# Performance work log

Measured on AMD Instinct MI355X. Metric: run time of the kernel, lower is better.

Reference implementation:

```python
import jax, jax.numpy as jnp
import numpy as np

N_AGENTS = 32
UNIT_DIM = 32
STATE_DIM = 1200
N_HEAD = 8
EMBED = 64
KEY_HID = 2 * EMBED
HYPER = 256
V_HID = 4 * EMBED
ATTEND_REG_COEF = 0.001
BS, T = 128, 32


def setup_inputs() -> dict:
    key = jax.random.key(0)
    ks = jax.random.split(key, 12)
    def lin(k, shape, fan_in):
        return jax.random.normal(k, shape, jnp.float32) / np.sqrt(fan_in)
    return dict(
        agent_qs=jax.random.normal(ks[0], (BS, T, N_AGENTS), jnp.float32),
        states=jax.random.normal(ks[1], (BS, T, STATE_DIM), jnp.float32),
        actions=jax.random.randint(ks[2], (BS, T, N_AGENTS), 0, 20),
        sel_W1=lin(ks[3], (N_HEAD, HYPER, STATE_DIM), STATE_DIM),
        sel_b1=jnp.zeros((N_HEAD, HYPER), jnp.float32),
        sel_W2=lin(ks[4], (N_HEAD, EMBED, HYPER), HYPER),
        key_W1=lin(ks[5], (N_HEAD, KEY_HID, UNIT_DIM + 1), UNIT_DIM + 1),
        key_b1=jnp.zeros((N_HEAD, KEY_HID), jnp.float32),
        key_W2=lin(ks[6], (N_HEAD, EMBED, KEY_HID), KEY_HID),
        wh_W1=lin(ks[7], (HYPER, STATE_DIM), STATE_DIM),
        wh_b1=jnp.zeros((HYPER,), jnp.float32),
        wh_W2=lin(ks[8], (N_HEAD, HYPER), HYPER),
        wh_b2=jnp.zeros((N_HEAD,), jnp.float32),
        v_W1=lin(ks[9], (V_HID, STATE_DIM), STATE_DIM),
        v_b1=jnp.zeros((V_HID,), jnp.float32),
        v_W2=lin(ks[10], (1, V_HID), V_HID),
        v_b2=jnp.zeros((1,), jnp.float32),
    )


def reference(agent_qs, states, actions, sel_W1, sel_b1, sel_W2, key_W1, key_b1, key_W2,
              wh_W1, wh_b1, wh_W2, wh_b2, v_W1, v_b1, v_W2, v_b2):
    bs = agent_qs.shape[0]
    s = states.reshape(-1, STATE_DIM)                       # (B, S), B = bs*T
    B = s.shape[0]
    units = s[:, :UNIT_DIM * N_AGENTS].reshape(B, N_AGENTS, UNIT_DIM)  # (B, A, U)
    q = agent_qs.reshape(B, N_AGENTS)                       # (B, A)
    # nonlinear=True: append each agent's q to its unit features
    units = jnp.concatenate([units, q[:, :, None]], axis=2)  # (B, A, U+1)
    a = actions.reshape(B, N_AGENTS)
    # selector hypernets (all heads batched): (B, H, E)
    h1 = jax.nn.relu(jnp.einsum('bs,hes->bhe', s, sel_W1) + sel_b1[None])
    sel = jnp.einsum('bhe,hde->bhd', h1, sel_W2)
    # key hypernets (all heads x all agents batched): (B, H, A, E)
    k1 = jax.nn.relu(jnp.einsum('bau,hku->bhak', units, key_W1) + key_b1[None, :, None, :])
    keys = jnp.einsum('bhak,hdk->bhad', k1, key_W2)
    logits = jnp.einsum('bhd,bhad->bha', sel, keys)          # unscaled, used for regularizer
    scaled = logits / np.sqrt(EMBED)
    scaled = jnp.where(a[:, None, :] == 0, -99999999.0, scaled)  # mask_dead
    w = jax.nn.softmax(scaled, axis=2)                       # (B, H, A)
    head_q = jnp.einsum('ba,bha->bh', q, w)                  # (B, H)
    # weighted_head + state_bias
    wh = jnp.abs(jax.nn.relu(s @ wh_W1.T + wh_b1) @ wh_W2.T + wh_b2)  # (B, H)
    v = (jax.nn.relu(s @ v_W1.T + v_b1) @ v_W2.T + v_b2)[:, 0]        # (B,)
    y = (wh * head_q).sum(axis=1) + v
    q_tot = y.reshape(bs, -1, 1)
    # sum over heads of per-head mean of squared (unscaled) logits
    attend_mag_regs = ATTEND_REG_COEF * (logits ** 2).mean(axis=(0, 2)).sum()
    # per-head entropy: sum over agents, mean over batch
    head_entropies = -(jnp.log(w + 1e-8) * w).sum(axis=2).mean(axis=0)  # (H,)
    return q_tot, attend_mag_regs, head_entropies
```

## Files before the change

### kernel.cpp

```cpp
#include <hip/hip_runtime.h>

#define B_TOT 4096
#define SDIM  1200
#define KPAD  1216
#define NA    32
#define NH    8
#define EMB   64
#define KHID  128
#define HYP   256
#define NSEL  2048
#define NTOT  2560

#define WS_H1BF 0
#define WS_M    (WS_H1BF + (size_t)B_TOT * NTOT / 2)
#define WS_LG   (WS_M    + (size_t)B_TOT * NH * KHID)
#define WS_PART (WS_LG   + (size_t)B_TOT * NH * NA)
#define WS_P2   (WS_PART + (size_t)B_TOT * 16)
#define WS_ABF  (WS_P2   + (size_t)32 * 16)
#define WS_WBF  (WS_ABF  + (size_t)B_TOT * KPAD / 2)
#define WS_KW32 (WS_WBF  + (size_t)NTOT * KPAD / 2)
#define WS_W32F (WS_KW32 + (size_t)1024 * 32 / 2)
#define WS_M2T  (WS_W32F + (size_t)1024)
#define WS_UBF  (WS_M2T  + (size_t)NH * KHID * HYP / 2)

typedef __attribute__((ext_vector_type(8))) short short8v;
typedef __attribute__((ext_vector_type(4))) float floatx4;

#define GLL16(gsrc, ldst) __builtin_amdgcn_global_load_lds( \
    (const __attribute__((address_space(1))) unsigned int*)(gsrc), \
    (__attribute__((address_space(3))) unsigned int*)(ldst), 16, 0, 0)

__device__ __forceinline__ ushort f2bf(float x) {
    unsigned u = __builtin_bit_cast(unsigned, x);
    unsigned r = (u + 0x7FFFu + ((u >> 16) & 1u)) >> 16;
    return (ushort)r;
}
__device__ __forceinline__ float bf2f(ushort u) {
    unsigned x = ((unsigned)u) << 16;
    return __builtin_bit_cast(float, x);
}

__global__ __launch_bounds__(256) void k_cvt_states(
    const float* __restrict__ src, ushort* __restrict__ dst)
{
    const size_t g = (size_t)blockIdx.x * 256 + threadIdx.x;
    if (g >= (size_t)B_TOT * (KPAD / 4)) return;
    const int row = (int)(g / (KPAD / 4));
    const int c4  = (int)(g % (KPAD / 4)) * 4;
    ushort4 o = {0, 0, 0, 0};
    if (c4 < SDIM) {
        float4 v = *(const float4*)(src + (size_t)row * SDIM + c4);
        o.x = f2bf(v.x); o.y = f2bf(v.y); o.z = f2bf(v.z); o.w = f2bf(v.w);
    }
    *(ushort4*)(dst + (size_t)row * KPAD + c4) = o;
}

__global__ __launch_bounds__(256) void k_cvt_w(
    const float* __restrict__ sel_W1, const float* __restrict__ wh_W1,
    const float* __restrict__ v_W1, ushort* __restrict__ dst)
{
    const size_t g = (size_t)blockIdx.x * 256 + threadIdx.x;
    if (g >= (size_t)NTOT * (KPAD / 4)) return;
    const int row = (int)(g / (KPAD / 4));
    const int c4  = (int)(g % (KPAD / 4)) * 4;
    const float* src = (row < NSEL)       ? (sel_W1 + (size_t)row * SDIM)
                     : (row < NSEL + HYP) ? (wh_W1 + (size_t)(row - NSEL) * SDIM)
                                          : (v_W1  + (size_t)(row - NSEL - HYP) * SDIM);
    ushort4 o = {0, 0, 0, 0};
    if (c4 < SDIM) {
        float4 v = *(const float4*)(src + c4);
        o.x = f2bf(v.x); o.y = f2bf(v.y); o.z = f2bf(v.z); o.w = f2bf(v.w);
    }
    *(ushort4*)(dst + (size_t)row * KPAD + c4) = o;
}

__global__ __launch_bounds__(256) void k_cvt_units(
    const float* __restrict__ states, ushort* __restrict__ dst)
{
    const int row = blockIdx.x * 256 + threadIdx.x;
    if (row >= B_TOT * NA) return;
    const int b = row >> 5, a = row & 31;
    const float* s = states + (size_t)b * SDIM + a * 32;
    ushort o[32];
    #pragma unroll
    for (int j = 0; j < 8; ++j) {
        float4 v = *(const float4*)(s + j * 4);
        o[j * 4 + 0] = f2bf(v.x); o[j * 4 + 1] = f2bf(v.y);
        o[j * 4 + 2] = f2bf(v.z); o[j * 4 + 3] = f2bf(v.w);
    }
    #pragma unroll
    for (int c = 0; c < 4; ++c)
        *(short8v*)(dst + (size_t)row * 32 + c * 8) = *(short8v*)&o[c * 8];
}

__global__ __launch_bounds__(256) void k_cvt_kw2(
    const float* __restrict__ key_W1, ushort* __restrict__ kw32,
    float* __restrict__ w32f)
{
    const int row = blockIdx.x * 256 + threadIdx.x;
    if (row >= 1024) return;
    const float* srcr = key_W1 + (size_t)row * 33;
    ushort o[32];
    #pragma unroll
    for (int u = 0; u < 32; ++u) o[u] = f2bf(srcr[u]);
    #pragma unroll
    for (int c = 0; c < 4; ++c)
        *(short8v*)(kw32 + (size_t)row * 32 + c * 8) = *(short8v*)&o[c * 8];
    w32f[row] = srcr[32];
}

__global__ __launch_bounds__(256) void k_m2(
    const float* __restrict__ sel_W2, const float* __restrict__ key_W2,
    ushort* __restrict__ M2T)
{
    __shared__ float ssel[EMB * HYP];
    __shared__ float skey[EMB][8];
    const int t  = threadIdx.x;
    const int h  = blockIdx.x;
    const int k0 = blockIdx.y * 8;

    const float4* sw = (const float4*)(sel_W2 + (size_t)h * EMB * HYP);
    #pragma unroll
    for (int j = 0; j < 16; ++j)
        ((float4*)ssel)[j * 256 + t] = sw[j * 256 + t];
    if (t < EMB) {
        #pragma unroll
        for (int kk = 0; kk < 8; ++kk)
            skey[t][kk] = key_W2[((size_t)h * EMB + t) * KHID + k0 + kk];
    }
    __syncthreads();

    const int e = t;
    float acc[8] = {};
    for (int d = 0; d < EMB; ++d) {
        const float sv = ssel[d * HYP + e];
        #pragma unroll
        for (int kk = 0; kk < 8; ++kk)
            acc[kk] = fmaf(sv, skey[d][kk], acc[kk]);
    }
    #pragma unroll
    for (int kk = 0; kk < 8; ++kk)
        M2T[((size_t)h * KHID + k0 + kk) * HYP + e] = f2bf(acc[kk]);
}

#define BK 32
__global__ __launch_bounds__(256) void k_gemm1_mfma(
    const ushort* __restrict__ Abf, const ushort* __restrict__ Wbf,
    const float* __restrict__ sel_b1, const float* __restrict__ wh_b1,
    const float* __restrict__ v_b1, ushort* __restrict__ h1bf)
{
    __shared__ ushort As[128 * BK];
    __shared__ ushort Bs[128 * BK];
    const int tid = threadIdx.x;
    const int l   = tid & 63;
    const int w   = tid >> 6;
    const int wM  = w >> 1, wN = w & 1;
    const int arow0 = blockIdx.y * 128;
    const int nrow0 = blockIdx.x * 128;

    const int srow = tid >> 2;
    const int skof = (tid & 3) * 8;
    const ushort* gA = Abf + (size_t)(arow0 + srow) * KPAD + skof;
    const ushort* gB = Wbf + (size_t)(nrow0 + srow) * KPAD + skof;
    ushort* lA = &As[srow * BK + skof];
    ushort* lB = &Bs[srow * BK + skof];

    floatx4 acc[4][4] = {};

    for (int k0 = 0; k0 < KPAD; k0 += BK) {
        GLL16(gA + k0, lA);
        GLL16(gA + (size_t)64 * KPAD + k0, lA + 64 * BK);
        GLL16(gB + k0, lB);
        GLL16(gB + (size_t)64 * KPAD + k0, lB + 64 * BK);
        __syncthreads();

        const int kch = (l >> 4) * 8;
        short8v av[4], bv[4];
        #pragma unroll
        for (int mi = 0; mi < 4; ++mi)
            av[mi] = *(const short8v*)&As[(wM * 64 + mi * 16 + (l & 15)) * BK + kch];
        #pragma unroll
        for (int ni = 0; ni < 4; ++ni)
            bv[ni] = *(const short8v*)&Bs[(wN * 64 + ni * 16 + (l & 15)) * BK + kch];
        #pragma unroll
        for (int mi = 0; mi < 4; ++mi)
            #pragma unroll
            for (int ni = 0; ni < 4; ++ni)
                acc[mi][ni] = __builtin_amdgcn_mfma_f32_16x16x32_bf16(
                    av[mi], bv[ni], acc[mi][ni], 0, 0, 0);
        __syncthreads();
    }

    float bias_n[4];
    #pragma unroll
    for (int ni = 0; ni < 4; ++ni) {
        const int col = nrow0 + wN * 64 + ni * 16 + (l & 15);
        bias_n[ni] = (col < NSEL)       ? sel_b1[col]
                   : (col < NSEL + HYP) ? wh_b1[col - NSEL]
                                        : v_b1[col - NSEL - HYP];
    }
    #pragma unroll
    for (int mi = 0; mi < 4; ++mi) {
        const int row = arow0 + wM * 64 + mi * 16 + (l >> 4) * 4;
        #pragma unroll
        for (int ni = 0; ni < 4; ++ni) {
            const int col = nrow0 + wN * 64 + ni * 16 + (l & 15);
            #pragma unroll
            for (int r = 0; r < 4; ++r)
                h1bf[(size_t)(row + r) * NTOT + col] =
                    f2bf(fmaxf(acc[mi][ni][r] + bias_n[ni], 0.f));
        }
    }
}

__global__ __launch_bounds__(256) void k_m_mfma(
    const ushort* __restrict__ h1bf, const ushort* __restrict__ M2T,
    float* __restrict__ m_out)
{
    __shared__ ushort As[128 * BK];
    __shared__ ushort Bs[128 * BK];
    const int tid = threadIdx.x;
    const int l   = tid & 63;
    const int w   = tid >> 6;
    const int wM  = w >> 1, wN = w & 1;
    const int h     = blockIdx.x;
    const int brow0 = blockIdx.y * 128;

    const int srow = tid >> 2;
    const int skof = (tid & 3) * 8;
    const ushort* gA = h1bf + (size_t)(brow0 + srow) * NTOT + h * HYP + skof;
    const ushort* gB = M2T + ((size_t)h * KHID + srow) * HYP + skof;
    ushort* lA = &As[srow * BK + skof];
    ushort* lB = &Bs[srow * BK + skof];

    floatx4 acc[4][4] = {};

    for (int k0 = 0; k0 < HYP; k0 += BK) {
        GLL16(gA + k0, lA);
        GLL16(gA + (size_t)64 * NTOT + k0, lA + 64 * BK);
        GLL16(gB + k0, lB);
        GLL16(gB + (size_t)64 * HYP + k0, lB + 64 * BK);
        __syncthreads();

        const int kch = (l >> 4) * 8;
        short8v av[4], bv[4];
        #pragma unroll
        for (int mi = 0; mi < 4; ++mi)
            av[mi] = *(const short8v*)&As[(wM * 64 + mi * 16 + (l & 15)) * BK + kch];
        #pragma unroll
        for (int ni = 0; ni < 4; ++ni)
            bv[ni] = *(const short8v*)&Bs[(wN * 64 + ni * 16 + (l & 15)) * BK + kch];
        #pragma unroll
        for (int mi = 0; mi < 4; ++mi)
            #pragma unroll
            for (int ni = 0; ni < 4; ++ni)
                acc[mi][ni] = __builtin_amdgcn_mfma_f32_16x16x32_bf16(
                    av[mi], bv[ni], acc[mi][ni], 0, 0, 0);
        __syncthreads();
    }

    #pragma unroll
    for (int mi = 0; mi < 4; ++mi) {
        const int row = brow0 + wM * 64 + mi * 16 + (l >> 4) * 4;
        #pragma unroll
        for (int ni = 0; ni < 4; ++ni) {
            const int col = wN * 64 + ni * 16 + (l & 15);
            #pragma unroll
            for (int r = 0; r < 4; ++r)
                m_out[((size_t)(row + r) * NH + h) * KHID + col] = acc[mi][ni][r];
        }
    }
}

__global__ __launch_bounds__(256) void k_logits_mfma(
    const ushort* __restrict__ Ubf, const ushort* __restrict__ KW32,
    const float* __restrict__ W32f, const float* __restrict__ key_b1,
    const float* __restrict__ agent_qs, const float* __restrict__ m_in,
    float* __restrict__ logits)
{
    const int tid = threadIdx.x;
    const int l   = tid & 63;
    const int w   = tid >> 6;
    const int b   = blockIdx.x * 4 + w;
    const int urow0 = b * NA;

    short8v av[2];
    float4 qv[2];
    #pragma unroll
    for (int mi = 0; mi < 2; ++mi) {
        av[mi] = *(const short8v*)(
            Ubf + (size_t)(urow0 + mi * 16 + (l & 15)) * 32 + (l >> 4) * 8);
        qv[mi] = *(const float4*)(
            agent_qs + (size_t)b * NA + mi * 16 + (l >> 4) * 4);
    }

    for (int h = 0; h < NH; ++h) {
        short8v bv[8];
        float b1r[8], w32r[8], mr[8];
        #pragma unroll
        for (int ni = 0; ni < 8; ++ni) {
            const int k = ni * 16 + (l & 15);
            bv[ni]   = *(const short8v*)(
                KW32 + ((size_t)h * KHID + k) * 32 + (l >> 4) * 8);
            b1r[ni]  = key_b1[h * KHID + k];
            w32r[ni] = W32f[h * KHID + k];
            mr[ni]   = m_in[((size_t)b * NH + h) * KHID + k];
        }
        floatx4 acc[2][8] = {};
        #pragma unroll
        for (int mi = 0; mi < 2; ++mi)
            #pragma unroll
            for (int ni = 0; ni < 8; ++ni)
                acc[mi][ni] = __builtin_amdgcn_mfma_f32_16x16x32_bf16(
                    av[mi], bv[ni], acc[mi][ni], 0, 0, 0);

        #pragma unroll
        for (int mi = 0; mi < 2; ++mi) {
            float s0 = 0.f, s1 = 0.f, s2 = 0.f, s3 = 0.f;
            #pragma unroll
            for (int ni = 0; ni < 8; ++ni) {
                const float b1v = b1r[ni], wv = w32r[ni], mv = mr[ni];
                s0 = fmaf(fmaxf(fmaf(qv[mi].x, wv, acc[mi][ni][0] + b1v), 0.f), mv, s0);
                s1 = fmaf(fmaxf(fmaf(qv[mi].y, wv, acc[mi][ni][1] + b1v), 0.f), mv, s1);
                s2 = fmaf(fmaxf(fmaf(qv[mi].z, wv, acc[mi][ni][2] + b1v), 0.f), mv, s2);
                s3 = fmaf(fmaxf(fmaf(qv[mi].w, wv, acc[mi][ni][3] + b1v), 0.f), mv, s3);
            }
            #pragma unroll
            for (int off = 8; off >= 1; off >>= 1) {
                s0 += __shfl_xor(s0, off);
                s1 += __shfl_xor(s1, off);
                s2 += __shfl_xor(s2, off);
                s3 += __shfl_xor(s3, off);
            }
            if ((l & 15) == 0) {
                float4 o = {s0, s1, s2, s3};
                *(float4*)(logits + ((size_t)b * NH + h) * NA
                           + mi * 16 + (l >> 4) * 4) = o;
            }
        }
    }
}

__global__ __launch_bounds__(256) void k_softmax(
    const float* __restrict__ logits, const float* __restrict__ agent_qs,
    const int* __restrict__ actions, const ushort* __restrict__ h1bf,
    const float* __restrict__ wh_W2, const float* __restrict__ wh_b2,
    const float* __restrict__ v_W2, const float* __restrict__ v_b2,
    float* __restrict__ out, float* __restrict__ part)
{
    __shared__ float qs[NA];
    __shared__ int   act_s[NA];
    __shared__ float whs[NH];
    __shared__ float hq[NH];
    __shared__ float vred[4];
    const int b = blockIdx.x, t = threadIdx.x;
    if (t < NA) {
        qs[t]    = agent_qs[(size_t)b * NA + t];
        act_s[t] = actions[(size_t)b * NA + t];
    }
    const int h = t >> 5, a = t & 31;
    {
        float acc = 0.f;
        #pragma unroll
        for (int j = 0; j < 8; ++j) {
            const int e = a + 32 * j;
            acc = fmaf(bf2f(h1bf[(size_t)b * NTOT + NSEL + e]),
                       wh_W2[h * HYP + e], acc);
        }
        #pragma unroll
        for (int off = 16; off >= 1; off >>= 1) acc += __shfl_xor(acc, off, 32);
        if (a == 0) whs[h] = fabsf(acc + wh_b2[h]);
    }
    {
        float acc = bf2f(h1bf[(size_t)b * NTOT + NSEL + HYP + t]) * v_W2[t];
        #pragma unroll
        for (int off = 32; off >= 1; off >>= 1) acc += __shfl_xor(acc, off);
        if ((t & 63) == 0) vred[t >> 6] = acc;
    }
    __syncthreads();

    const float lg = logits[((size_t)b * NH + h) * NA + a];
    float sc = (act_s[a] == 0) ? -99999999.0f : lg * 0.125f;

    float mx = sc;
    #pragma unroll
    for (int off = 16; off >= 1; off >>= 1) mx = fmaxf(mx, __shfl_xor(mx, off, 32));
    const float e = expf(sc - mx);
    float sum = e;
    #pragma unroll
    for (int off = 16; off >= 1; off >>= 1) sum += __shfl_xor(sum, off, 32);
    const float wgt = e / sum;

    float r_sq  = lg * lg;
    float r_hq  = qs[a] * wgt;
    float r_ent = -wgt * logf(wgt + 1e-8f);
    #pragma unroll
    for (int off = 16; off >= 1; off >>= 1) {
        r_sq  += __shfl_xor(r_sq,  off, 32);
        r_hq  += __shfl_xor(r_hq,  off, 32);
        r_ent += __shfl_xor(r_ent, off, 32);
    }
    if (a == 0) {
        hq[h] = r_hq;
        part[(size_t)b * 16 + h]     = r_sq;
        part[(size_t)b * 16 + 8 + h] = r_ent;
    }
    __syncthreads();
    if (t == 0) {
        float y = vred[0] + vred[1] + vred[2] + vred[3] + v_b2[0];
        #pragma unroll
        for (int i = 0; i < NH; ++i) y = fmaf(whs[i], hq[i], y);
        out[b] = y;
    }
}

__global__ __launch_bounds__(256) void k_final_s1(
    const float* __restrict__ part, float* __restrict__ part2)
{
    __shared__ float red[16][17];
    const int t = threadIdx.x;
    const int c = t & 15, rl = t >> 4;
    const int rbase = blockIdx.x * 128 + rl;
    float v0 = 0.f, v1 = 0.f, v2 = 0.f, v3 = 0.f;
    #pragma unroll
    for (int j = 0; j < 8; j += 4) {
        v0 += part[(size_t)(rbase + (j + 0) * 16) * 16 + c];
        v1 += part[(size_t)(rbase + (j + 1) * 16) * 16 + c];
        v2 += part[(size_t)(rbase + (j + 2) * 16) * 16 + c];
        v3 += part[(size_t)(rbase + (j + 3) * 16) * 16 + c];
    }
    red[rl][c] = (v0 + v1) + (v2 + v3);
    __syncthreads();
    if (t < 16) {
        float s = 0.f;
        #pragma unroll
        for (int i = 0; i < 16; ++i) s += red[i][t];
        part2[blockIdx.x * 16 + t] = s;
    }
}

__global__ __launch_bounds__(256) void k_final_s2(
    const float* __restrict__ part2, float* __restrict__ out)
{
    __shared__ float red[16][17];
    __shared__ float tot[16];
    const int t = threadIdx.x;
    {
        const int g = t >> 4, c = t & 15;
        red[g][c] = part2[t] + part2[t + 256];
    }
    __syncthreads();
    if (t < 16) {
        float s = 0.f;
        #pragma unroll
        for (int i = 0; i < 16; ++i) s += red[i][t];
        tot[t] = s;
    }
    __syncthreads();
    if (t == 0) {
        float s = 0.f;
        #pragma unroll
        for (int i = 0; i < 8; ++i) s += tot[i];
        out[B_TOT] = 0.001f * (s / (float)((size_t)B_TOT * NA));
    }
    if (t >= 8 && t < 16)
        out[B_TOT + 1 + (t - 8)] = tot[t] / (float)B_TOT;
}

extern "C" void kernel_launch(void* const* d_in, const int* in_sizes, int n_in,
                              void* d_out, int out_size, void* d_ws, size_t ws_size,
                              hipStream_t stream) {
    (void)in_sizes; (void)n_in; (void)out_size; (void)ws_size;
    const float* agent_qs = (const float*)d_in[0];
    const float* states   = (const float*)d_in[1];
    const int*   actions  = (const int*)d_in[2];
    const float* sel_W1   = (const float*)d_in[3];
    const float* sel_b1   = (const float*)d_in[4];
    const float* sel_W2   = (const float*)d_in[5];
    const float* key_W1   = (const float*)d_in[6];
    const float* key_b1   = (const float*)d_in[7];
    const float* key_W2   = (const float*)d_in[8];
    const float* wh_W1    = (const float*)d_in[9];
    const float* wh_b1    = (const float*)d_in[10];
    const float* wh_W2    = (const float*)d_in[11];
    const float* wh_b2    = (const float*)d_in[12];
    const float* v_W1     = (const float*)d_in[13];
    const float* v_b1     = (const float*)d_in[14];
    const float* v_W2     = (const float*)d_in[15];
    const float* v_b2     = (const float*)d_in[16];

    float* out = (float*)d_out;
    float* ws  = (float*)d_ws;
    ushort* h1bf  = (ushort*)(ws + WS_H1BF);
    float* m_buf  = ws + WS_M;
    float* lg_buf = ws + WS_LG;
    float* part   = ws + WS_PART;
    float* part2  = ws + WS_P2;
    ushort* Abf   = (ushort*)(ws + WS_ABF);
    ushort* Wbf   = (ushort*)(ws + WS_WBF);
    ushort* KW32  = (ushort*)(ws + WS_KW32);
    float*  W32f  = ws + WS_W32F;
    ushort* M2T   = (ushort*)(ws + WS_M2T);
    ushort* Ubf   = (ushort*)(ws + WS_UBF);

    {
        const int groups_a = B_TOT * (KPAD / 4);
        const int groups_w = NTOT * (KPAD / 4);
        k_cvt_states<<<(groups_a + 255) / 256, 256, 0, stream>>>(states, Abf);
        k_cvt_w<<<(groups_w + 255) / 256, 256, 0, stream>>>(sel_W1, wh_W1, v_W1, Wbf);
        k_cvt_kw2<<<4, 256, 0, stream>>>(key_W1, KW32, W32f);
        k_cvt_units<<<(B_TOT * NA + 255) / 256, 256, 0, stream>>>(states, Ubf);
        k_m2<<<dim3(NH, KHID / 8), 256, 0, stream>>>(sel_W2, key_W2, M2T);
    }
    k_gemm1_mfma<<<dim3(NTOT / 128, B_TOT / 128), 256, 0, stream>>>(
        Abf, Wbf, sel_b1, wh_b1, v_b1, h1bf);
    k_m_mfma<<<dim3(NH, B_TOT / 128), 256, 0, stream>>>(h1bf, M2T, m_buf);
    k_logits_mfma<<<dim3(B_TOT / 4), 256, 0, stream>>>(
        Ubf, KW32, W32f, key_b1, agent_qs, m_buf, lg_buf);
    k_softmax<<<dim3(B_TOT), 256, 0, stream>>>(
        lg_buf, agent_qs, actions, h1bf, wh_W2, wh_b2, v_W2, v_b2, out, part);
    k_final_s1<<<32, 256, 0, stream>>>(part, part2);
    k_final_s2<<<1, 256, 0, stream>>>(part2, out);
}
```

Before: 123.1 us.

## Double-buffer GEMM LDS tiles, store m in bf16, shrink m tiles, reuse bf16 states

```diff
diff --git a/kernel.cpp b/kernel.cpp
--- a/kernel.cpp
+++ b/kernel.cpp
@@ -12,8 +12,8 @@
 #define NTOT  2560
 
 #define WS_H1BF 0
-#define WS_M    (WS_H1BF + (size_t)B_TOT * NTOT / 2)
-#define WS_LG   (WS_M    + (size_t)B_TOT * NH * KHID)
+#define WS_MBF  (WS_H1BF + (size_t)B_TOT * NTOT / 2)
+#define WS_LG   (WS_MBF  + (size_t)B_TOT * NH * KHID / 2)
 #define WS_PART (WS_LG   + (size_t)B_TOT * NH * NA)
 #define WS_P2   (WS_PART + (size_t)B_TOT * 16)
 #define WS_ABF  (WS_P2   + (size_t)32 * 16)
@@ -75,22 +75,20 @@
 }
 
 __global__ __launch_bounds__(256) void k_cvt_units(
-    const float* __restrict__ states, ushort* __restrict__ dst)
+    const ushort* __restrict__ Abf, ushort* __restrict__ dst)
 {
     const int row = blockIdx.x * 256 + threadIdx.x;
     if (row >= B_TOT * NA) return;
     const int b = row >> 5, a = row & 31;
-    const float* s = states + (size_t)b * SDIM + a * 32;
-    ushort o[32];
-    #pragma unroll
-    for (int j = 0; j < 8; ++j) {
-        float4 v = *(const float4*)(s + j * 4);
-        o[j * 4 + 0] = f2bf(v.x); o[j * 4 + 1] = f2bf(v.y);
-        o[j * 4 + 2] = f2bf(v.z); o[j * 4 + 3] = f2bf(v.w);
-    }
-    #pragma unroll
-    for (int c = 0; c < 4; ++c)
-        *(short8v*)(dst + (size_t)row * 32 + c * 8) = *(short8v*)&o[c * 8];
+    const ushort* s = Abf + (size_t)b * KPAD + a * 32;
+    short8v v0 = *(const short8v*)(s);
+    short8v v1 = *(const short8v*)(s + 8);
+    short8v v2 = *(const short8v*)(s + 16);
+    short8v v3 = *(const short8v*)(s + 24);
+    *(short8v*)(dst + (size_t)row * 32)      = v0;
+    *(short8v*)(dst + (size_t)row * 32 + 8)  = v1;
+    *(short8v*)(dst + (size_t)row * 32 + 16) = v2;
+    *(short8v*)(dst + (size_t)row * 32 + 24) = v3;
 }
 
 __global__ __launch_bounds__(256) void k_cvt_kw2(
@@ -149,8 +147,8 @@
     const float* __restrict__ sel_b1, const float* __restrict__ wh_b1,
     const float* __restrict__ v_b1, ushort* __restrict__ h1bf)
 {
-    __shared__ ushort As[128 * BK];
-    __shared__ ushort Bs[128 * BK];
+    __shared__ ushort As[2][128 * BK];
+    __shared__ ushort Bs[2][128 * BK];
     const int tid = threadIdx.x;
     const int l   = tid & 63;
     const int w   = tid >> 6;
@@ -162,26 +160,30 @@
     const int skof = (tid & 3) * 8;
     const ushort* gA = Abf + (size_t)(arow0 + srow) * KPAD + skof;
     const ushort* gB = Wbf + (size_t)(nrow0 + srow) * KPAD + skof;
-    ushort* lA = &As[srow * BK + skof];
-    ushort* lB = &Bs[srow * BK + skof];
+
+#define STAGE_G1(BUF, KK) do { \
+    GLL16(gA + (KK), &As[BUF][srow * BK + skof]); \
+    GLL16(gA + (size_t)64 * KPAD + (KK), &As[BUF][(64 + srow) * BK + skof]); \
+    GLL16(gB + (KK), &Bs[BUF][srow * BK + skof]); \
+    GLL16(gB + (size_t)64 * KPAD + (KK), &Bs[BUF][(64 + srow) * BK + skof]); \
+} while (0)
 
     floatx4 acc[4][4] = {};
 
+    STAGE_G1(0, 0);
+    __syncthreads();
+    int cur = 0;
     for (int k0 = 0; k0 < KPAD; k0 += BK) {
-        GLL16(gA + k0, lA);
-        GLL16(gA + (size_t)64 * KPAD + k0, lA + 64 * BK);
-        GLL16(gB + k0, lB);
-        GLL16(gB + (size_t)64 * KPAD + k0, lB + 64 * BK);
-        __syncthreads();
+        if (k0 + BK < KPAD) STAGE_G1(cur ^ 1, k0 + BK);
 
         const int kch = (l >> 4) * 8;
         short8v av[4], bv[4];
         #pragma unroll
         for (int mi = 0; mi < 4; ++mi)
-            av[mi] = *(const short8v*)&As[(wM * 64 + mi * 16 + (l & 15)) * BK + kch];
+            av[mi] = *(const short8v*)&As[cur][(wM * 64 + mi * 16 + (l & 15)) * BK + kch];
         #pragma unroll
         for (int ni = 0; ni < 4; ++ni)
-            bv[ni] = *(const short8v*)&Bs[(wN * 64 + ni * 16 + (l & 15)) * BK + kch];
+            bv[ni] = *(const short8v*)&Bs[cur][(wN * 64 + ni * 16 + (l & 15)) * BK + kch];
         #pragma unroll
         for (int mi = 0; mi < 4; ++mi)
             #pragma unroll
@@ -189,6 +191,7 @@
                 acc[mi][ni] = __builtin_amdgcn_mfma_f32_16x16x32_bf16(
                     av[mi], bv[ni], acc[mi][ni], 0, 0, 0);
         __syncthreads();
+        cur ^= 1;
     }
 
     float bias_n[4];
@@ -215,59 +218,64 @@
 
 __global__ __launch_bounds__(256) void k_m_mfma(
     const ushort* __restrict__ h1bf, const ushort* __restrict__ M2T,
-    float* __restrict__ m_out)
-{
-    __shared__ ushort As[128 * BK];
-    __shared__ ushort Bs[128 * BK];
+    ushort* __restrict__ m_out)
+{
+    __shared__ ushort As[2][64 * BK];
+    __shared__ ushort Bs[2][128 * BK];
     const int tid = threadIdx.x;
     const int l   = tid & 63;
     const int w   = tid >> 6;
     const int wM  = w >> 1, wN = w & 1;
     const int h     = blockIdx.x;
-    const int brow0 = blockIdx.y * 128;
+    const int brow0 = blockIdx.y * 64;
 
     const int srow = tid >> 2;
     const int skof = (tid & 3) * 8;
     const ushort* gA = h1bf + (size_t)(brow0 + srow) * NTOT + h * HYP + skof;
     const ushort* gB = M2T + ((size_t)h * KHID + srow) * HYP + skof;
-    ushort* lA = &As[srow * BK + skof];
-    ushort* lB = &Bs[srow * BK + skof];
-
-    floatx4 acc[4][4] = {};
-
+
+#define STAGE_M(BUF, KK) do { \
+    GLL16(gA + (KK), &As[BUF][srow * BK + skof]); \
+    GLL16(gB + (KK), &Bs[BUF][srow * BK + skof]); \
+    GLL16(gB + (size_t)64 * HYP + (KK), &Bs[BUF][(64 + srow) * BK + skof]); \
+} while (0)
+
+    floatx4 acc[2][4] = {};
+
+    STAGE_M(0, 0);
+    __syncthreads();
+    int cur = 0;
     for (int k0 = 0; k0 < HYP; k0 += BK) {
-        GLL16(gA + k0, lA);
-        GLL16(gA + (size_t)64 * NTOT + k0, lA + 64 * BK);
-        GLL16(gB + k0, lB);
-        GLL16(gB + (size_t)64 * HYP + k0, lB + 64 * BK);
-        __syncthreads();
+        if (k0 + BK < HYP) STAGE_M(cur ^ 1, k0 + BK);
 
         const int kch = (l >> 4) * 8;
-        short8v av[4], bv[4];
-        #pragma unroll
-        for (int mi = 0; mi < 4; ++mi)
-            av[mi] = *(const short8v*)&As[(wM * 64 + mi * 16 + (l & 15)) * BK + kch];
+        short8v av[2], bv[4];
+        #pragma unroll
+        for (int mi = 0; mi < 2; ++mi)
+            av[mi] = *(const short8v*)&As[cur][(wM * 32 + mi * 16 + (l & 15)) * BK + kch];
         #pragma unroll
         for (int ni = 0; ni < 4; ++ni)
-            bv[ni] = *(const short8v*)&Bs[(wN * 64 + ni * 16 + (l & 15)) * BK + kch];
-        #pragma unroll
-        for (int mi = 0; mi < 4; ++mi)
+            bv[ni] = *(const short8v*)&Bs[cur][(wN * 64 + ni * 16 + (l & 15)) * BK + kch];
+        #pragma unroll
+        for (int mi = 0; mi < 2; ++mi)
             #pragma unroll
             for (int ni = 0; ni < 4; ++ni)
                 acc[mi][ni] = __builtin_amdgcn_mfma_f32_16x16x32_bf16(
                     av[mi], bv[ni], acc[mi][ni], 0, 0, 0);
         __syncthreads();
-    }
-
-    #pragma unroll
-    for (int mi = 0; mi < 4; ++mi) {
-        const int row = brow0 + wM * 64 + mi * 16 + (l >> 4) * 4;
+        cur ^= 1;
+    }
+
+    #pragma unroll
+    for (int mi = 0; mi < 2; ++mi) {
+        const int row = brow0 + wM * 32 + mi * 16 + (l >> 4) * 4;
         #pragma unroll
         for (int ni = 0; ni < 4; ++ni) {
             const int col = wN * 64 + ni * 16 + (l & 15);
             #pragma unroll
             for (int r = 0; r < 4; ++r)
-                m_out[((size_t)(row + r) * NH + h) * KHID + col] = acc[mi][ni][r];
+                m_out[((size_t)(row + r) * NH + h) * KHID + col] =
+                    f2bf(acc[mi][ni][r]);
         }
     }
 }
@@ -275,7 +283,7 @@
 __global__ __launch_bounds__(256) void k_logits_mfma(
     const ushort* __restrict__ Ubf, const ushort* __restrict__ KW32,
     const float* __restrict__ W32f, const float* __restrict__ key_b1,
-    const float* __restrict__ agent_qs, const float* __restrict__ m_in,
+    const float* __restrict__ agent_qs, const ushort* __restrict__ m_in,
     float* __restrict__ logits)
 {
     const int tid = threadIdx.x;
@@ -304,7 +312,7 @@
                 KW32 + ((size_t)h * KHID + k) * 32 + (l >> 4) * 8);
             b1r[ni]  = key_b1[h * KHID + k];
             w32r[ni] = W32f[h * KHID + k];
-            mr[ni]   = m_in[((size_t)b * NH + h) * KHID + k];
+            mr[ni]   = bf2f(m_in[((size_t)b * NH + h) * KHID + k]);
         }
         floatx4 acc[2][8] = {};
         #pragma unroll
@@ -492,7 +500,7 @@
     float* out = (float*)d_out;
     float* ws  = (float*)d_ws;
     ushort* h1bf  = (ushort*)(ws + WS_H1BF);
-    float* m_buf  = ws + WS_M;
+    ushort* m_buf = (ushort*)(ws + WS_MBF);
     float* lg_buf = ws + WS_LG;
     float* part   = ws + WS_PART;
     float* part2  = ws + WS_P2;
@@ -509,12 +517,12 @@
         k_cvt_states<<<(groups_a + 255) / 256, 256, 0, stream>>>(states, Abf);
         k_cvt_w<<<(groups_w + 255) / 256, 256, 0, stream>>>(sel_W1, wh_W1, v_W1, Wbf);
         k_cvt_kw2<<<4, 256, 0, stream>>>(key_W1, KW32, W32f);
-        k_cvt_units<<<(B_TOT * NA + 255) / 256, 256, 0, stream>>>(states, Ubf);
+        k_cvt_units<<<(B_TOT * NA + 255) / 256, 256, 0, stream>>>(Abf, Ubf);
         k_m2<<<dim3(NH, KHID / 8), 256, 0, stream>>>(sel_W2, key_W2, M2T);
     }
     k_gemm1_mfma<<<dim3(NTOT / 128, B_TOT / 128), 256, 0, stream>>>(
         Abf, Wbf, sel_b1, wh_b1, v_b1, h1bf);
-    k_m_mfma<<<dim3(NH, B_TOT / 128), 256, 0, stream>>>(h1bf, M2T, m_buf);
+    k_m_mfma<<<dim3(NH, B_TOT / 64), 256, 0, stream>>>(h1bf, M2T, m_buf);
     k_logits_mfma<<<dim3(B_TOT / 4), 256, 0, stream>>>(
         Ubf, KW32, W32f, key_b1, agent_qs, m_buf, lg_buf);
     k_softmax<<<dim3(B_TOT), 256, 0, stream>>>(
```

New measurement: 123.7 us. Within noise of the previous version (+0.5%).
